# Kernel tuning notes

Measured on AMD Instinct MI355X. Metric: run time of the kernel, lower is better.

Reference implementation:

```python
import jax, jax.numpy as jnp
import numpy as np

B, T, D_IN, H = 2048, 240, 180, 90


def setup_inputs() -> dict:
    key = jax.random.key(0)
    k1, k2, k3, k4, k5 = jax.random.split(key, 5)
    s = 1.0 / np.sqrt(H)  # torch LSTMCell init scale
    return {
        "x": jax.random.normal(k1, (B, 3, 60, 240), dtype=jnp.float32),
        "W_ih": jax.random.uniform(k2, (4 * H, D_IN), dtype=jnp.float32, minval=-s, maxval=s),
        "W_hh": jax.random.uniform(k3, (4 * H, H), dtype=jnp.float32, minval=-s, maxval=s),
        "b_ih": jax.random.uniform(k4, (4 * H,), dtype=jnp.float32, minval=-s, maxval=s),
        "b_hh": jax.random.uniform(k5, (4 * H,), dtype=jnp.float32, minval=-s, maxval=s),
    }


def reference(x, W_ih, W_hh, b_ih, b_hh):
    # (B, 3, 60, 240) -> (B, 240, 3, 60) -> (B, 240, 180)
    b = x.shape[0]
    xt = jnp.transpose(x, (0, 3, 1, 2)).reshape(b, T, D_IN)
    # NOTE: the torch module calls LSTMCell without carrying state, so h0=c0=0
    # at EVERY timestep; the W_hh contribution is identically zero and all
    # timesteps are independent -> one batched GEMM over (B*T).
    gates = jnp.einsum("bti,gi->btg", xt, W_ih) + b_ih + b_hh  # (B, T, 4H)
    i_g, f_g, g_g, o_g = jnp.split(gates, 4, axis=-1)  # torch gate order i,f,g,o
    c = jax.nn.sigmoid(i_g) * jnp.tanh(g_g)  # f_g * c_prev = 0
    h = jax.nn.sigmoid(o_g) * jnp.tanh(c)
    return jax.nn.sigmoid(h)  # (B, T, H)
```

## Files before the change

### kernel.cpp

```cpp
#include <hip/hip_runtime.h>


#define B_SZ 2048
#define T_SZ 240
#define K_SZ 180
#define H_SZ 90
#define KP   192
#define TB   80
#define NP   3
#define NTT  5

#define WS_B_OFF 110592

typedef __bf16 bf16x8 __attribute__((ext_vector_type(8)));
typedef __bf16 bf16x4 __attribute__((ext_vector_type(4)));
typedef float  f32x4  __attribute__((ext_vector_type(4)));

__device__ __forceinline__ float sigmoidf_(float x) {
    return __builtin_amdgcn_rcpf(1.0f + __expf(-x));
}
__device__ __forceinline__ float tanhf_(float x) {
    return 1.0f - 2.0f * __builtin_amdgcn_rcpf(__expf(2.0f * x) + 1.0f);
}

__device__ __forceinline__ int skey(int t) {
    return (2 * (t + (t >> 4))) & 14;
}
__device__ __forceinline__ int sgran(int g, int t) {
    return (g & ~15) | ((g ^ skey(t)) & 15);
}

__global__ __launch_bounds__(384) void prepack_kernel(
    const float* __restrict__ W_ih,
    const float* __restrict__ b_ih,
    const float* __restrict__ b_hh,
    void* __restrict__ ws)
{
    __bf16* wp = (__bf16*)ws;
    float*  bp = (float*)((char*)ws + WS_B_OFF);
    const int gb[3] = {0, 180, 270};

    const int bid = blockIdx.x;
    const int tid = threadIdx.x;
    if (bid < 18) {
        const int g  = bid / 6;
        const int ks = bid % 6;
        const int w  = tid >> 6;
        const int l  = tid & 63;
        const int q  = l >> 4;
        const int n  = l & 15;
        const int h  = w * 16 + n;
        bf16x8 f;
        #pragma unroll
        for (int j = 0; j < 8; ++j) {
            int k = ks * 32 + q * 8 + j;
            float v = (h < H_SZ && k < K_SZ) ? W_ih[(size_t)(gb[g] + h) * K_SZ + k] : 0.0f;
            f[j] = (__bf16)v;
        }
        *(bf16x8*)(wp + (size_t)(((g * 6 + ks) * 6 + w) * 64 + l) * 8) = f;
    } else {
        if (tid < 288) {
            int g = tid / 96, hh = tid % 96;
            bp[g * 96 + hh] = (hh < H_SZ) ? (b_ih[gb[g] + hh] + b_hh[gb[g] + hh]) : 0.0f;
        }
    }
}

__global__ __launch_bounds__(384, 5) void lstm_fused_kernel(
    const float* __restrict__ x,
    const void*  __restrict__ ws,
    float* __restrict__ out)
{
    __shared__ __align__(16) __bf16 aBuf[TB * KP];

    const int bid  = blockIdx.x;
    const int b    = bid / NP;
    const int part = bid - b * NP;
    const int t0   = part * TB;

    const int tid  = threadIdx.x;
    const int wave = tid >> 6;
    const int lane = tid & 63;
    const int q    = lane >> 4;
    const int n    = lane & 15;
    const int h    = wave * 16 + n;
    const bool hv  = (h < H_SZ);

    const float* xb = x + (size_t)b * (K_SZ * T_SZ) + t0;

    if (tid < TB * 3) {
        int t  = tid / 3;
        int gz = 45 + (tid - (tid / 3) * 3);
        *(unsigned long long*)(aBuf + t * KP + sgran(gz, t) * 4) = 0ull;
    }

    #pragma unroll
    for (int p = 0; p < 3; ++p) {
        int u = tid + p * 384;
        if (p < 2 || u < 900) {
            int k4 = u / 20;
            int t4 = u - k4 * 20;
            const float* src = xb + (k4 * 4) * T_SZ + t4 * 4;
            f32x4 r0 = *(const f32x4*)(src);
            f32x4 r1 = *(const f32x4*)(src + T_SZ);
            f32x4 r2 = *(const f32x4*)(src + 2 * T_SZ);
            f32x4 r3 = *(const f32x4*)(src + 3 * T_SZ);
            #pragma unroll
            for (int j = 0; j < 4; ++j) {
                int t = t4 * 4 + j;
                bf16x4 w;
                w[0] = (__bf16)r0[j]; w[1] = (__bf16)r1[j];
                w[2] = (__bf16)r2[j]; w[3] = (__bf16)r3[j];
                *(bf16x4*)(aBuf + t * KP + sgran(k4, t) * 4) = w;
            }
        }
    }
    __syncthreads();

    const bf16x8* wp = (const bf16x8*)ws;

    f32x4 acc[NTT][3];
    #pragma unroll
    for (int tt = 0; tt < NTT; ++tt)
        #pragma unroll
        for (int g = 0; g < 3; ++g)
            acc[tt][g] = (f32x4){0.f, 0.f, 0.f, 0.f};

    #pragma unroll
    for (int ks = 0; ks < 6; ++ks) {
        bf16x8 b0 = wp[((0 * 6 + ks) * 6 + wave) * 64 + lane];
        bf16x8 b1 = wp[((1 * 6 + ks) * 6 + wave) * 64 + lane];
        bf16x8 b2 = wp[((2 * 6 + ks) * 6 + wave) * 64 + lane];
        #pragma unroll
        for (int tt = 0; tt < NTT; ++tt) {
            int t = tt * 16 + n;
            int g = ks * 8 + 2 * q;
            bf16x8 a = *(const bf16x8*)(aBuf + t * KP + sgran(g, t) * 4);
            acc[tt][0] = __builtin_amdgcn_mfma_f32_16x16x32_bf16(a, b0, acc[tt][0], 0, 0, 0);
            acc[tt][1] = __builtin_amdgcn_mfma_f32_16x16x32_bf16(a, b1, acc[tt][1], 0, 0, 0);
            acc[tt][2] = __builtin_amdgcn_mfma_f32_16x16x32_bf16(a, b2, acc[tt][2], 0, 0, 0);
        }
    }

    const float* bp = (const float*)((const char*)ws + WS_B_OFF);
    const float bias_i = bp[0 * 96 + h];
    const float bias_g = bp[1 * 96 + h];
    const float bias_o = bp[2 * 96 + h];
    float* ob = out + (size_t)b * (T_SZ * H_SZ) + (size_t)t0 * H_SZ;

    if (hv) {
        #pragma unroll
        for (int tt = 0; tt < NTT; ++tt) {
            #pragma unroll
            for (int e = 0; e < 4; ++e) {
                float gi = acc[tt][0][e] + bias_i;
                float gg = acc[tt][1][e] + bias_g;
                float go = acc[tt][2][e] + bias_o;
                float cc = sigmoidf_(gi) * tanhf_(gg);
                float hh = sigmoidf_(go) * tanhf_(cc);
                ob[(size_t)(tt * 16 + q * 4 + e) * H_SZ + h] = sigmoidf_(hh);
            }
        }
    }
}

extern "C" void kernel_launch(void* const* d_in, const int* in_sizes, int n_in,
                              void* d_out, int out_size, void* d_ws, size_t ws_size,
                              hipStream_t stream) {
    const float* x    = (const float*)d_in[0];
    const float* W_ih = (const float*)d_in[1];
    const float* b_ih = (const float*)d_in[3];
    const float* b_hh = (const float*)d_in[4];
    float* out = (float*)d_out;

    prepack_kernel<<<dim3(19), dim3(384), 0, stream>>>(W_ih, b_ih, b_hh, d_ws);
    lstm_fused_kernel<<<dim3(B_SZ * NP), dim3(384), 0, stream>>>(x, d_ws, out);
}
```

Before: 662.9 us.

## Preload weight fragments and interleave per-tile MFMA with epilogue stores

Loads all weight fragments into registers before the shared-memory barrier so their global latency overlaps with the x staging. Reorders the loop nest so each time tile's GEMM is followed immediately by its activation and stores, which shrinks live accumulators and spreads stores across the kernel. Adds a workgroup barrier between tiles, presumably to keep waves in lockstep. Lowers the launch-bounds occupancy hint from 5 to 3 to accommodate the extra fragment registers, at the cost of fewer resident blocks for hiding memory latency.

```diff
diff --git a/kernel.cpp b/kernel.cpp
--- a/kernel.cpp
+++ b/kernel.cpp
@@ -66,7 +66,7 @@
     }
 }
 
-__global__ __launch_bounds__(384, 5) void lstm_fused_kernel(
+__global__ __launch_bounds__(384, 3) void lstm_fused_kernel(
     const float* __restrict__ x,
     const void*  __restrict__ ws,
     float* __restrict__ out)
@@ -115,32 +115,14 @@
             }
         }
     }
-    __syncthreads();
 
     const bf16x8* wp = (const bf16x8*)ws;
-
-    f32x4 acc[NTT][3];
+    bf16x8 bfrag[3][6];
     #pragma unroll
-    for (int tt = 0; tt < NTT; ++tt)
+    for (int g = 0; g < 3; ++g)
         #pragma unroll
-        for (int g = 0; g < 3; ++g)
-            acc[tt][g] = (f32x4){0.f, 0.f, 0.f, 0.f};
-
-    #pragma unroll
-    for (int ks = 0; ks < 6; ++ks) {
-        bf16x8 b0 = wp[((0 * 6 + ks) * 6 + wave) * 64 + lane];
-        bf16x8 b1 = wp[((1 * 6 + ks) * 6 + wave) * 64 + lane];
-        bf16x8 b2 = wp[((2 * 6 + ks) * 6 + wave) * 64 + lane];
-        #pragma unroll
-        for (int tt = 0; tt < NTT; ++tt) {
-            int t = tt * 16 + n;
-            int g = ks * 8 + 2 * q;
-            bf16x8 a = *(const bf16x8*)(aBuf + t * KP + sgran(g, t) * 4);
-            acc[tt][0] = __builtin_amdgcn_mfma_f32_16x16x32_bf16(a, b0, acc[tt][0], 0, 0, 0);
-            acc[tt][1] = __builtin_amdgcn_mfma_f32_16x16x32_bf16(a, b1, acc[tt][1], 0, 0, 0);
-            acc[tt][2] = __builtin_amdgcn_mfma_f32_16x16x32_bf16(a, b2, acc[tt][2], 0, 0, 0);
-        }
-    }
+        for (int ks = 0; ks < 6; ++ks)
+            bfrag[g][ks] = wp[((g * 6 + ks) * 6 + wave) * 64 + lane];
 
     const float* bp = (const float*)((const char*)ws + WS_B_OFF);
     const float bias_i = bp[0 * 96 + h];
@@ -148,19 +130,35 @@
     const float bias_o = bp[2 * 96 + h];
     float* ob = out + (size_t)b * (T_SZ * H_SZ) + (size_t)t0 * H_SZ;
 
-    if (hv) {
+    __syncthreads();
+
+    #pragma unroll
+    for (int tt = 0; tt < NTT; ++tt) {
+        f32x4 acc0 = {0.f, 0.f, 0.f, 0.f};
+        f32x4 acc1 = {0.f, 0.f, 0.f, 0.f};
+        f32x4 acc2 = {0.f, 0.f, 0.f, 0.f};
+        const int t = tt * 16 + n;
         #pragma unroll
-        for (int tt = 0; tt < NTT; ++tt) {
+        for (int ks = 0; ks < 6; ++ks) {
+            int g = ks * 8 + 2 * q;
+            bf16x8 a = *(const bf16x8*)(aBuf + t * KP + sgran(g, t) * 4);
+            acc0 = __builtin_amdgcn_mfma_f32_16x16x32_bf16(a, bfrag[0][ks], acc0, 0, 0, 0);
+            acc1 = __builtin_amdgcn_mfma_f32_16x16x32_bf16(a, bfrag[1][ks], acc1, 0, 0, 0);
+            acc2 = __builtin_amdgcn_mfma_f32_16x16x32_bf16(a, bfrag[2][ks], acc2, 0, 0, 0);
+        }
+        if (hv) {
+            const int tg = tt * 16 + q * 4;
             #pragma unroll
             for (int e = 0; e < 4; ++e) {
-                float gi = acc[tt][0][e] + bias_i;
-                float gg = acc[tt][1][e] + bias_g;
-                float go = acc[tt][2][e] + bias_o;
+                float gi = acc0[e] + bias_i;
+                float gg = acc1[e] + bias_g;
+                float go = acc2[e] + bias_o;
                 float cc = sigmoidf_(gi) * tanhf_(gg);
                 float hh = sigmoidf_(go) * tanhf_(cc);
-                ob[(size_t)(tt * 16 + q * 4 + e) * H_SZ + h] = sigmoidf_(hh);
+                ob[(size_t)(tg + e) * H_SZ + h] = sigmoidf_(hh);
             }
         }
+        if (tt + 1 < NTT) __builtin_amdgcn_s_barrier();
     }
 }
 
```

After: 554.5 us (median of 3 runs). -16.4%, faster.
